# Kernel tuning notes

Measured on AMD Instinct MI355X. Metric: run time of the kernel, lower is better.

The kernel has to match this reference:

```python
import jax, jax.numpy as jnp
import numpy as np

H = 128          # input hidden dim
HID = 128        # expert hidden width
OUT = 128        # out_channels
NR = 8           # n_routed
NS = 2           # n_shared
RDIM = 16        # router feature dim


def setup_inputs() -> dict:
    key = jax.random.key(0)
    ks = jax.random.split(key, 11)
    s = 0.05
    x = jax.random.normal(ks[0], (2, 32, 32, 32, H), dtype=jnp.float32)
    # router params
    Wr1 = jax.random.normal(ks[1], (H, RDIM), dtype=jnp.float32) * s
    br1 = jnp.zeros((RDIM,), dtype=jnp.float32)
    Wr2 = jax.random.normal(ks[2], (RDIM, NR), dtype=jnp.float32) * s
    br2 = jnp.zeros((NR,), dtype=jnp.float32)
    # routed expert params, stacked on leading expert axis
    We1 = jax.random.normal(ks[3], (NR, H, HID), dtype=jnp.float32) * s
    be1 = jnp.zeros((NR, HID), dtype=jnp.float32)
    We2 = jax.random.normal(ks[4], (NR, HID, OUT), dtype=jnp.float32) * s
    be2 = jnp.zeros((NR, OUT), dtype=jnp.float32)
    # shared expert params
    Ws1 = jax.random.normal(ks[5], (NS, H, HID), dtype=jnp.float32) * s
    bs1 = jnp.zeros((NS, HID), dtype=jnp.float32)
    Ws2 = jax.random.normal(ks[6], (NS, HID, OUT), dtype=jnp.float32) * s
    bs2 = jnp.zeros((NS, OUT), dtype=jnp.float32)
    return dict(x=x, Wr1=Wr1, br1=br1, Wr2=Wr2, br2=br2,
                We1=We1, be1=be1, We2=We2, be2=be2,
                Ws1=Ws1, bs1=bs1, Ws2=Ws2, bs2=bs2)


def reference(x, Wr1, br1, Wr2, br2, We1, be1, We2, be2, Ws1, bs1, Ws2, bs2):
    # router: Dense(16) -> relu -> Dense(n_routed) -> softmax
    rf = jax.nn.relu(jnp.einsum('...h,hr->...r', x, Wr1) + br1)
    logits = jnp.einsum('...r,re->...e', rf, Wr2) + br2
    gate = jax.nn.softmax(logits, axis=-1)                      # [..., NR]
    threshold = 1.0 / NR
    mask = (gate > threshold).astype(gate.dtype)
    mg = gate * mask
    mg = mg / (jnp.sum(mg, axis=-1, keepdims=True) + 1e-8)
    # routed experts (batched over expert axis e): Dense -> gelu(tanh) -> Dense
    hr = jax.nn.gelu(jnp.einsum('...h,ehd->...ed', x, We1) + be1)   # [..., NR, HID]
    ro = jnp.einsum('...ed,edo->...eo', hr, We2) + be2              # [..., NR, OUT]
    routed_agg = jnp.einsum('...eo,...e->...o', ro, mg)
    # shared experts summed
    hs = jax.nn.gelu(jnp.einsum('...h,ehd->...ed', x, Ws1) + bs1)   # [..., NS, HID]
    so = jnp.einsum('...ed,edo->...eo', hs, Ws2) + bs2              # [..., NS, OUT]
    shared_agg = jnp.sum(so, axis=-2)
    return routed_agg + shared_agg
```

## Files before the change

### kernel.cpp

```cpp
#include <hip/hip_runtime.h>
#include <hip/hip_bf16.h>

typedef __bf16 bf16x8 __attribute__((ext_vector_type(8)));
typedef __bf16 bf16x4 __attribute__((ext_vector_type(4)));
typedef float  f32x16 __attribute__((ext_vector_type(16)));
typedef float  f32x4  __attribute__((ext_vector_type(4)));

static __device__ __forceinline__ f32x16 mfma32(bf16x8 a, bf16x8 b, f32x16 c) {
    return __builtin_amdgcn_mfma_f32_32x32x16_bf16(a, b, c, 0, 0, 0);
}

__global__ __launch_bounds__(256) void pack_kernel(
    const float* __restrict__ We1, const float* __restrict__ Ws1,
    const float* __restrict__ We2, const float* __restrict__ Ws2,
    __bf16* __restrict__ w1p, __bf16* __restrict__ w2p)
{
    int idx = blockIdx.x * 256 + threadIdx.x;
    int which = idx / 20480;
    int tid = idx - which * 20480;
    int l  = tid & 63;
    int ks = (tid >> 6) & 7;
    int nt = (tid >> 9) & 3;
    int e  = tid >> 11;
    const float* src;
    __bf16* dst;
    if (which == 0) {
        src = (e < 8) ? (We1 + e * 16384) : (Ws1 + (e - 8) * 16384);
        dst = w1p;
    } else {
        src = (e < 8) ? (We2 + e * 16384) : (Ws2 + (e - 8) * 16384);
        dst = w2p;
    }
    int col  = nt * 32 + (l & 31);
    int krow = ks * 16 + (l >> 5) * 8;
    bf16x8 v;
    #pragma unroll
    for (int j = 0; j < 8; ++j)
        v[j] = (__bf16)src[(krow + j) * 128 + col];
    *(bf16x8*)(dst + (((e * 4 + nt) * 8 + ks) * 64 + l) * 8) = v;
}

__global__ __launch_bounds__(256) void router_kernel(
    const float* __restrict__ x,
    const float* __restrict__ Wr1, const float* __restrict__ br1,
    const float* __restrict__ Wr2, const float* __restrict__ br2,
    float* __restrict__ mg)
{
    int tok = blockIdx.x * 256 + threadIdx.x;
    const float* xr = x + (size_t)tok * 128;
    double rf[16];
    #pragma unroll
    for (int r = 0; r < 16; ++r) rf[r] = (double)br1[r];
    #pragma unroll 4
    for (int k = 0; k < 128; ++k) {
        double xv = (double)xr[k];
        #pragma unroll
        for (int r = 0; r < 16; ++r)
            rf[r] = fma(xv, (double)Wr1[k * 16 + r], rf[r]);
    }
    #pragma unroll
    for (int r = 0; r < 16; ++r) rf[r] = rf[r] > 0.0 ? rf[r] : 0.0;
    double lg[8];
    #pragma unroll
    for (int j = 0; j < 8; ++j) lg[j] = (double)br2[j];
    #pragma unroll
    for (int r = 0; r < 16; ++r) {
        double rv = rf[r];
        #pragma unroll
        for (int j = 0; j < 8; ++j)
            lg[j] = fma(rv, (double)Wr2[r * 8 + j], lg[j]);
    }
    double mx = lg[0];
    #pragma unroll
    for (int j = 1; j < 8; ++j) mx = lg[j] > mx ? lg[j] : mx;
    double ex[8]; double s = 0.0;
    #pragma unroll
    for (int j = 0; j < 8; ++j) { ex[j] = exp(lg[j] - mx); s += ex[j]; }
    double mv[8]; double ms = 0.0;
    #pragma unroll
    for (int j = 0; j < 8; ++j) {
        double g = ex[j] / s;
        double m = (g > 0.125) ? g : 0.0;
        mv[j] = m; ms += m;
    }
    double inv = 1.0 / (ms + 1e-8);
    f32x4 o0, o1;
    o0[0]=(float)(mv[0]*inv); o0[1]=(float)(mv[1]*inv);
    o0[2]=(float)(mv[2]*inv); o0[3]=(float)(mv[3]*inv);
    o1[0]=(float)(mv[4]*inv); o1[1]=(float)(mv[5]*inv);
    o1[2]=(float)(mv[6]*inv); o1[3]=(float)(mv[7]*inv);
    f32x4* op = (f32x4*)(mg + (size_t)tok * 8);
    op[0] = o0; op[1] = o1;
}

__global__ __launch_bounds__(256, 2) void moe_main_kernel(
    const float* __restrict__ x, const float* __restrict__ mg,
    const __bf16* __restrict__ w1p, const __bf16* __restrict__ w2p,
    const float* __restrict__ be1, const float* __restrict__ bs1,
    const float* __restrict__ be2, const float* __restrict__ bs2,
    float* __restrict__ out)
{
    __shared__ __align__(16) __bf16 Xp[16384];
    __shared__ __align__(16) __bf16 Hp[16384];

    const int t    = threadIdx.x;
    const int lane = t & 63;
    const int wave = t >> 6;
    const int l31  = lane & 31;
    const int lh   = lane >> 5;
    const int tok0 = blockIdx.x * 128;
    const int ntp  = (wave & 1) * 2;
    const int mtp  = (wave >> 1) * 2;

    #pragma unroll
    for (int i = 0; i < 8; ++i) {
        int g = i * 256 + t;
        int m = g >> 4;
        int c = g & 15;
        const f32x4* srcp = (const f32x4*)(x + (size_t)(tok0 + m) * 128 + c * 8);
        f32x4 va = srcp[0], vb = srcp[1];
        bf16x8 v;
        v[0]=(__bf16)va[0]; v[1]=(__bf16)va[1]; v[2]=(__bf16)va[2]; v[3]=(__bf16)va[3];
        v[4]=(__bf16)vb[0]; v[5]=(__bf16)vb[1]; v[6]=(__bf16)vb[2]; v[7]=(__bf16)vb[3];
        *(bf16x8*)&Xp[(((m >> 5) * 8 + (c >> 1)) * 64 + (c & 1) * 32 + (m & 31)) * 8] = v;
    }
    __syncthreads();

    f32x16 acc[2][2];
    #pragma unroll
    for (int i0 = 0; i0 < 2; ++i0)
        #pragma unroll
        for (int i1 = 0; i1 < 2; ++i1)
            #pragma unroll
            for (int i = 0; i < 16; ++i) acc[i0][i1][i] = 0.f;

    #pragma unroll 1
    for (int e = 0; e < 10; ++e) {
        float gate0 = 1.f, gate1 = 1.f;
        if (e < 8) {
            gate0 = mg[(size_t)(tok0 + (mtp + 0) * 32 + l31) * 8 + e];
            gate1 = mg[(size_t)(tok0 + (mtp + 1) * 32 + l31) * 8 + e];
        }
        const float* b1p = (e < 8) ? (be1 + e * 128) : (bs1 + (e - 8) * 128);

        const __bf16* w1b = w1p + (size_t)e * 16384;
        bf16x8 wf[2][8];
        #pragma unroll
        for (int n2 = 0; n2 < 2; ++n2)
            #pragma unroll
            for (int ks = 0; ks < 8; ++ks)
                wf[n2][ks] = *(const bf16x8*)(w1b + (((ntp + n2) * 8 + ks) * 64 + lane) * 8);

        f32x16 a1[2][2];
        #pragma unroll
        for (int i0 = 0; i0 < 2; ++i0)
            #pragma unroll
            for (int i1 = 0; i1 < 2; ++i1)
                #pragma unroll
                for (int i = 0; i < 16; ++i) a1[i0][i1][i] = 0.f;

        #pragma unroll
        for (int ks = 0; ks < 8; ++ks) {
            bf16x8 xb0 = *(const bf16x8*)&Xp[(((mtp + 0) * 8 + ks) * 64 + lane) * 8];
            bf16x8 xb1 = *(const bf16x8*)&Xp[(((mtp + 1) * 8 + ks) * 64 + lane) * 8];
            a1[0][0] = mfma32(wf[0][ks], xb0, a1[0][0]);
            a1[0][1] = mfma32(wf[0][ks], xb1, a1[0][1]);
            a1[1][0] = mfma32(wf[1][ks], xb0, a1[1][0]);
            a1[1][1] = mfma32(wf[1][ks], xb1, a1[1][1]);
        }
        __syncthreads();

        #pragma unroll
        for (int n2 = 0; n2 < 2; ++n2) {
            const int ntile = ntp + n2;
            #pragma unroll
            for (int m2 = 0; m2 < 2; ++m2) {
                const int mtile = mtp + m2;
                const float gv = (m2 == 0) ? gate0 : gate1;
                #pragma unroll
                for (int gq = 0; gq < 4; ++gq) {
                    int n0 = ntile * 32 + gq * 8 + lh * 4;
                    f32x4 b1v = *(const f32x4*)(b1p + n0);
                    bf16x4 hv;
                    #pragma unroll
                    for (int q = 0; q < 4; ++q) {
                        float v = a1[n2][m2][gq * 4 + q] + b1v[q];
                        float u  = 1.5957691216f * fmaf(0.044715f * v, v * v, v);
                        float sg = 1.f / (1.f + __expf(-u));
                        hv[q] = (__bf16)(v * sg * gv);
                    }
                    *(bf16x4*)&Hp[((mtile * 8 + (n0 >> 4)) * 64 + ((n0 >> 3) & 1) * 32 + l31) * 8
                                  + (n0 & 7)] = hv;
                }
            }
        }
        __syncthreads();

        const __bf16* w2b = w2p + (size_t)e * 16384;
        #pragma unroll
        for (int o2 = 0; o2 < 2; ++o2)
            #pragma unroll
            for (int ks = 0; ks < 8; ++ks)
                wf[o2][ks] = *(const bf16x8*)(w2b + (((ntp + o2) * 8 + ks) * 64 + lane) * 8);

        #pragma unroll
        for (int ks = 0; ks < 8; ++ks) {
            bf16x8 h0 = *(const bf16x8*)&Hp[(((mtp + 0) * 8 + ks) * 64 + lane) * 8];
            bf16x8 h1 = *(const bf16x8*)&Hp[(((mtp + 1) * 8 + ks) * 64 + lane) * 8];
            acc[0][0] = mfma32(h0, wf[0][ks], acc[0][0]);
            acc[0][1] = mfma32(h0, wf[1][ks], acc[0][1]);
            acc[1][0] = mfma32(h1, wf[0][ks], acc[1][0]);
            acc[1][1] = mfma32(h1, wf[1][ks], acc[1][1]);
        }
    }

    float be2c[2][8], bs2c[2];
    #pragma unroll
    for (int o2 = 0; o2 < 2; ++o2) {
        int o = (ntp + o2) * 32 + l31;
        #pragma unroll
        for (int ee = 0; ee < 8; ++ee) be2c[o2][ee] = be2[ee * 128 + o];
        bs2c[o2] = bs2[o] + bs2[128 + o];
    }
    const float* mgb = mg + (size_t)tok0 * 8;
    #pragma unroll
    for (int m2 = 0; m2 < 2; ++m2) {
        int mtile = mtp + m2;
        #pragma unroll
        for (int rg = 0; rg < 16; ++rg) {
            int mloc = mtile * 32 + 4 * lh + (rg & 3) + 8 * (rg >> 2);
            f32x4 g0 = *(const f32x4*)&mgb[mloc * 8];
            f32x4 g1 = *(const f32x4*)&mgb[mloc * 8 + 4];
            #pragma unroll
            for (int o2 = 0; o2 < 2; ++o2) {
                float b = bs2c[o2];
                #pragma unroll
                for (int ee = 0; ee < 4; ++ee) b = fmaf(g0[ee], be2c[o2][ee], b);
                #pragma unroll
                for (int ee = 0; ee < 4; ++ee) b = fmaf(g1[ee], be2c[o2][4 + ee], b);
                out[(size_t)(tok0 + mloc) * 128 + (ntp + o2) * 32 + l31] =
                    acc[m2][o2][rg] + b;
            }
        }
    }
}

extern "C" void kernel_launch(void* const* d_in, const int* in_sizes, int n_in,
                              void* d_out, int out_size, void* d_ws, size_t ws_size,
                              hipStream_t stream)
{
    const float* x   = (const float*)d_in[0];
    const float* Wr1 = (const float*)d_in[1];
    const float* br1 = (const float*)d_in[2];
    const float* Wr2 = (const float*)d_in[3];
    const float* br2 = (const float*)d_in[4];
    const float* We1 = (const float*)d_in[5];
    const float* be1 = (const float*)d_in[6];
    const float* We2 = (const float*)d_in[7];
    const float* be2 = (const float*)d_in[8];
    const float* Ws1 = (const float*)d_in[9];
    const float* bs1 = (const float*)d_in[10];
    const float* Ws2 = (const float*)d_in[11];
    const float* bs2 = (const float*)d_in[12];

    __bf16* w1p = (__bf16*)d_ws;
    __bf16* w2p = (__bf16*)((char*)d_ws + 327680);
    float*  mg  = (float*)((char*)d_ws + 655360);

    pack_kernel<<<160, 256, 0, stream>>>(We1, Ws1, We2, Ws2, w1p, w2p);
    router_kernel<<<256, 256, 0, stream>>>(x, Wr1, br1, Wr2, br2, mg);
    moe_main_kernel<<<512, 256, 0, stream>>>(x, mg, w1p, w2p, be1, bs1, be2, bs2,
                                             (float*)d_out);
}
```

Before: 205.8 us.

## Keep expert hidden activations in registers, fold bias into GEMM, split hidden across waves

The main kernel now chains the two expert GEMMs in registers. The first GEMM's accumulator layout is fed straight into the second GEMM's A operand, which removes the hidden-activation LDS round trip and its two barriers per expert. The first-layer bias is folded in as an extra K slice (a ones column in X, a bias row in the packed weights). Each wave pair splits the hidden dimension and reduces partial outputs through LDS at the end. GELU switches to an exp2/rcp form, and the router stages x through LDS with smaller blocks. This trades an extra K step and a final cross-wave reduction for fewer syncs and less LDS traffic, with tiles halved to 64 tokens per block.

```diff
diff --git a/kernel.cpp b/kernel.cpp
--- a/kernel.cpp
+++ b/kernel.cpp
@@ -2,61 +2,93 @@
 #include <hip/hip_bf16.h>
 
 typedef __bf16 bf16x8 __attribute__((ext_vector_type(8)));
-typedef __bf16 bf16x4 __attribute__((ext_vector_type(4)));
 typedef float  f32x16 __attribute__((ext_vector_type(16)));
 typedef float  f32x4  __attribute__((ext_vector_type(4)));
+typedef float  f32x2  __attribute__((ext_vector_type(2)));
 
 static __device__ __forceinline__ f32x16 mfma32(bf16x8 a, bf16x8 b, f32x16 c) {
     return __builtin_amdgcn_mfma_f32_32x32x16_bf16(a, b, c, 0, 0, 0);
 }
 
+#define GELU_C1 2.30220820f
+#define GELU_C2 0.10294324f
+
 __global__ __launch_bounds__(256) void pack_kernel(
-    const float* __restrict__ We1, const float* __restrict__ Ws1,
+    const float* __restrict__ We1, const float* __restrict__ be1,
+    const float* __restrict__ Ws1, const float* __restrict__ bs1,
     const float* __restrict__ We2, const float* __restrict__ Ws2,
     __bf16* __restrict__ w1p, __bf16* __restrict__ w2p)
 {
-    int idx = blockIdx.x * 256 + threadIdx.x;
-    int which = idx / 20480;
-    int tid = idx - which * 20480;
-    int l  = tid & 63;
-    int ks = (tid >> 6) & 7;
-    int nt = (tid >> 9) & 3;
-    int e  = tid >> 11;
-    const float* src;
-    __bf16* dst;
-    if (which == 0) {
-        src = (e < 8) ? (We1 + e * 16384) : (Ws1 + (e - 8) * 16384);
-        dst = w1p;
-    } else {
-        src = (e < 8) ? (We2 + e * 16384) : (Ws2 + (e - 8) * 16384);
-        dst = w2p;
-    }
-    int col  = nt * 32 + (l & 31);
-    int krow = ks * 16 + (l >> 5) * 8;
-    bf16x8 v;
-    #pragma unroll
-    for (int j = 0; j < 8; ++j)
-        v[j] = (__bf16)src[(krow + j) * 128 + col];
-    *(bf16x8*)(dst + (((e * 4 + nt) * 8 + ks) * 64 + l) * 8) = v;
-}
-
-__global__ __launch_bounds__(256) void router_kernel(
+    int tid = blockIdx.x * 256 + threadIdx.x;
+    if (tid < 23040) {
+        int l  = tid & 63;
+        int ks = (tid >> 6) % 9;
+        int nt = (tid / 576) & 3;
+        int e  = tid / 2304;
+        const float* src = (e < 8) ? (We1 + e * 16384) : (Ws1 + (e - 8) * 16384);
+        const float* bia = (e < 8) ? (be1 + e * 128)   : (bs1 + (e - 8) * 128);
+        int n = nt * 32 + (l & 31);
+        int kb = ks * 16 + (l >> 5) * 8;
+        bf16x8 v;
+        #pragma unroll
+        for (int j = 0; j < 8; ++j) {
+            int k = kb + j;
+            float f = (k < 128) ? src[k * 128 + n] : ((k == 128) ? bia[n] : 0.f);
+            v[j] = (__bf16)f;
+        }
+        *(bf16x8*)(w1p + (size_t)tid * 8) = v;
+    } else if (tid < 43520) {
+        int t2 = tid - 23040;
+        int l  = t2 & 63;
+        int ks = (t2 >> 6) & 7;
+        int ot = (t2 / 512) & 3;
+        int e  = t2 / 2048;
+        const float* src = (e < 8) ? (We2 + e * 16384) : (Ws2 + (e - 8) * 16384);
+        int o  = ot * 32 + (l & 31);
+        int lh = l >> 5;
+        bf16x8 v;
+        #pragma unroll
+        for (int j = 0; j < 8; ++j) {
+            int hid = 16 * ks + 8 * (j >> 2) + 4 * lh + (j & 3);
+            v[j] = (__bf16)src[hid * 128 + o];
+        }
+        *(bf16x8*)(w2p + (size_t)t2 * 8) = v;
+    }
+}
+
+__global__ __launch_bounds__(64) void router_kernel(
     const float* __restrict__ x,
     const float* __restrict__ Wr1, const float* __restrict__ br1,
     const float* __restrict__ Wr2, const float* __restrict__ br2,
     float* __restrict__ mg)
 {
-    int tok = blockIdx.x * 256 + threadIdx.x;
-    const float* xr = x + (size_t)tok * 128;
+    __shared__ __align__(16) float xs[64 * 132];
+    int t = threadIdx.x;
+    size_t base = (size_t)blockIdx.x * 64 * 128;
+    #pragma unroll 4
+    for (int i = 0; i < 32; ++i) {
+        int idx = i * 64 + t;
+        f32x4 v = *(const f32x4*)(x + base + (size_t)idx * 4);
+        int m = (idx * 4) >> 7;
+        int c = (idx * 4) & 127;
+        *(f32x4*)&xs[m * 132 + c] = v;
+    }
+    __syncthreads();
+
+    const f32x4* xr = (const f32x4*)(xs + t * 132);
     double rf[16];
     #pragma unroll
     for (int r = 0; r < 16; ++r) rf[r] = (double)br1[r];
-    #pragma unroll 4
-    for (int k = 0; k < 128; ++k) {
-        double xv = (double)xr[k];
-        #pragma unroll
-        for (int r = 0; r < 16; ++r)
-            rf[r] = fma(xv, (double)Wr1[k * 16 + r], rf[r]);
+    for (int c = 0; c < 32; ++c) {
+        f32x4 xv4 = xr[c];
+        #pragma unroll
+        for (int q = 0; q < 4; ++q) {
+            double xv = (double)xv4[q];
+            int k = c * 4 + q;
+            #pragma unroll
+            for (int r = 0; r < 16; ++r)
+                rf[r] = fma(xv, (double)Wr1[k * 16 + r], rf[r]);
+        }
     }
     #pragma unroll
     for (int r = 0; r < 16; ++r) rf[r] = rf[r] > 0.0 ? rf[r] : 0.0;
@@ -84,6 +116,7 @@
         mv[j] = m; ms += m;
     }
     double inv = 1.0 / (ms + 1e-8);
+    int tok = blockIdx.x * 64 + t;
     f32x4 o0, o1;
     o0[0]=(float)(mv[0]*inv); o0[1]=(float)(mv[1]*inv);
     o0[2]=(float)(mv[2]*inv); o0[3]=(float)(mv[3]*inv);
@@ -96,150 +129,152 @@
 __global__ __launch_bounds__(256, 2) void moe_main_kernel(
     const float* __restrict__ x, const float* __restrict__ mg,
     const __bf16* __restrict__ w1p, const __bf16* __restrict__ w2p,
-    const float* __restrict__ be1, const float* __restrict__ bs1,
     const float* __restrict__ be2, const float* __restrict__ bs2,
     float* __restrict__ out)
 {
-    __shared__ __align__(16) __bf16 Xp[16384];
-    __shared__ __align__(16) __bf16 Hp[16384];
+    __shared__ __align__(16) char lds[32768];
+    __bf16* Xp = (__bf16*)lds;
+    float*  Red = (float*)lds;
 
     const int t    = threadIdx.x;
     const int lane = t & 63;
     const int wave = t >> 6;
     const int l31  = lane & 31;
     const int lh   = lane >> 5;
-    const int tok0 = blockIdx.x * 128;
-    const int ntp  = (wave & 1) * 2;
-    const int mtp  = (wave >> 1) * 2;
-
-    #pragma unroll
-    for (int i = 0; i < 8; ++i) {
+    const int mt   = wave >> 1;
+    const int h    = wave & 1;
+    const int tok0 = blockIdx.x * 64;
+
+    #pragma unroll
+    for (int i = 0; i < 4; ++i) {
         int g = i * 256 + t;
         int m = g >> 4;
         int c = g & 15;
-        const f32x4* srcp = (const f32x4*)(x + (size_t)(tok0 + m) * 128 + c * 8);
-        f32x4 va = srcp[0], vb = srcp[1];
+        const f32x4* sp = (const f32x4*)(x + (size_t)(tok0 + m) * 128 + c * 8);
+        f32x4 va = sp[0], vb = sp[1];
         bf16x8 v;
         v[0]=(__bf16)va[0]; v[1]=(__bf16)va[1]; v[2]=(__bf16)va[2]; v[3]=(__bf16)va[3];
         v[4]=(__bf16)vb[0]; v[5]=(__bf16)vb[1]; v[6]=(__bf16)vb[2]; v[7]=(__bf16)vb[3];
-        *(bf16x8*)&Xp[(((m >> 5) * 8 + (c >> 1)) * 64 + (c & 1) * 32 + (m & 31)) * 8] = v;
+        *(bf16x8*)&Xp[(((m >> 5) * 9 + (c >> 1)) * 64 + (c & 1) * 32 + (m & 31)) * 8] = v;
+    }
+    if (t < 128) {
+        int mtx = t >> 6, l = t & 63;
+        bf16x8 v;
+        #pragma unroll
+        for (int j = 0; j < 8; ++j) v[j] = (__bf16)0.f;
+        if (l < 32) v[0] = (__bf16)1.0f;
+        *(bf16x8*)&Xp[((mtx * 9 + 8) * 64 + l) * 8] = v;
     }
     __syncthreads();
 
-    f32x16 acc[2][2];
-    #pragma unroll
-    for (int i0 = 0; i0 < 2; ++i0)
-        #pragma unroll
-        for (int i1 = 0; i1 < 2; ++i1)
-            #pragma unroll
-            for (int i = 0; i < 16; ++i) acc[i0][i1][i] = 0.f;
+    const float* mgr = mg + (size_t)(tok0 + 32 * mt + l31) * 8;
+    f32x4 ga4 = *(const f32x4*)mgr;
+    f32x4 gb4 = *(const f32x4*)(mgr + 4);
+    float gte[8] = {ga4[0], ga4[1], ga4[2], ga4[3], gb4[0], gb4[1], gb4[2], gb4[3]};
+
+    f32x16 acc[4];
+    #pragma unroll
+    for (int ot = 0; ot < 4; ++ot)
+        #pragma unroll
+        for (int i = 0; i < 16; ++i) acc[ot][i] = 0.f;
+
+    const bf16x8* w1v = (const bf16x8*)w1p;
+    const bf16x8* w2v = (const bf16x8*)w2p;
 
     #pragma unroll 1
     for (int e = 0; e < 10; ++e) {
-        float gate0 = 1.f, gate1 = 1.f;
-        if (e < 8) {
-            gate0 = mg[(size_t)(tok0 + (mtp + 0) * 32 + l31) * 8 + e];
-            gate1 = mg[(size_t)(tok0 + (mtp + 1) * 32 + l31) * 8 + e];
-        }
-        const float* b1p = (e < 8) ? (be1 + e * 128) : (bs1 + (e - 8) * 128);
-
-        const __bf16* w1b = w1p + (size_t)e * 16384;
-        bf16x8 wf[2][8];
+        const bf16x8* wap = w1v + ((size_t)(e * 4 + 2 * h) * 9) * 64 + lane;
+        bf16x8 wa[9], wb[9];
+        #pragma unroll
+        for (int ks = 0; ks < 9; ++ks) { wa[ks] = wap[ks * 64]; wb[ks] = wap[(9 + ks) * 64]; }
+
+        f32x16 a1[2];
         #pragma unroll
         for (int n2 = 0; n2 < 2; ++n2)
             #pragma unroll
-            for (int ks = 0; ks < 8; ++ks)
-                wf[n2][ks] = *(const bf16x8*)(w1b + (((ntp + n2) * 8 + ks) * 64 + lane) * 8);
-
-        f32x16 a1[2][2];
-        #pragma unroll
-        for (int i0 = 0; i0 < 2; ++i0)
-            #pragma unroll
-            for (int i1 = 0; i1 < 2; ++i1)
+            for (int i = 0; i < 16; ++i) a1[n2][i] = 0.f;
+
+        #pragma unroll
+        for (int ks = 0; ks < 9; ++ks) {
+            bf16x8 xb = *(const bf16x8*)&Xp[((mt * 9 + ks) * 64 + lane) * 8];
+            a1[0] = mfma32(wa[ks], xb, a1[0]);
+            a1[1] = mfma32(wb[ks], xb, a1[1]);
+        }
+
+        const bf16x8* wBp = w2v + ((size_t)(e * 4) * 8 + 4 * h) * 64 + lane;
+        bf16x8 wB[4][4];
+        #pragma unroll
+        for (int ot = 0; ot < 4; ++ot)
+            #pragma unroll
+            for (int kq = 0; kq < 4; ++kq)
+                wB[ot][kq] = wBp[(ot * 8 + kq) * 64];
+
+        const float gv = (e < 8) ? gte[e] : 1.0f;
+
+        #pragma unroll
+        for (int n2 = 0; n2 < 2; ++n2) {
+            #pragma unroll
+            for (int b = 0; b < 2; ++b) {
+                bf16x8 fr;
                 #pragma unroll
-                for (int i = 0; i < 16; ++i) a1[i0][i1][i] = 0.f;
-
-        #pragma unroll
-        for (int ks = 0; ks < 8; ++ks) {
-            bf16x8 xb0 = *(const bf16x8*)&Xp[(((mtp + 0) * 8 + ks) * 64 + lane) * 8];
-            bf16x8 xb1 = *(const bf16x8*)&Xp[(((mtp + 1) * 8 + ks) * 64 + lane) * 8];
-            a1[0][0] = mfma32(wf[0][ks], xb0, a1[0][0]);
-            a1[0][1] = mfma32(wf[0][ks], xb1, a1[0][1]);
-            a1[1][0] = mfma32(wf[1][ks], xb0, a1[1][0]);
-            a1[1][1] = mfma32(wf[1][ks], xb1, a1[1][1]);
-        }
-        __syncthreads();
-
-        #pragma unroll
-        for (int n2 = 0; n2 < 2; ++n2) {
-            const int ntile = ntp + n2;
-            #pragma unroll
-            for (int m2 = 0; m2 < 2; ++m2) {
-                const int mtile = mtp + m2;
-                const float gv = (m2 == 0) ? gate0 : gate1;
+                for (int jp = 0; jp < 4; ++jp) {
+                    f32x2 hh; hh[0] = a1[n2][8 * b + 2 * jp]; hh[1] = a1[n2][8 * b + 2 * jp + 1];
+                    f32x2 tt = hh * hh;
+                    f32x2 pp;
+                    pp[0] = fmaf(tt[0], -GELU_C2, -GELU_C1);
+                    pp[1] = fmaf(tt[1], -GELU_C2, -GELU_C1);
+                    f32x2 mm = hh * pp;
+                    float e0 = __builtin_amdgcn_exp2f(mm[0]);
+                    float e1 = __builtin_amdgcn_exp2f(mm[1]);
+                    float q0 = __builtin_amdgcn_rcpf(1.f + e0);
+                    float q1 = __builtin_amdgcn_rcpf(1.f + e1);
+                    f32x2 gg; gg[0] = hh[0] * q0 * gv; gg[1] = hh[1] * q1 * gv;
+                    fr[2 * jp]     = (__bf16)gg[0];
+                    fr[2 * jp + 1] = (__bf16)gg[1];
+                }
+                int kq = 2 * n2 + b;
+                acc[0] = mfma32(fr, wB[0][kq], acc[0]);
+                acc[1] = mfma32(fr, wB[1][kq], acc[1]);
+                acc[2] = mfma32(fr, wB[2][kq], acc[2]);
+                acc[3] = mfma32(fr, wB[3][kq], acc[3]);
+            }
+        }
+    }
+
+    __syncthreads();
+    if (h == 1) {
+        #pragma unroll
+        for (int ot = 0; ot < 4; ++ot)
+            #pragma unroll
+            for (int r = 0; r < 16; ++r)
+                Red[((mt * 4 + ot) * 16 + r) * 64 + lane] = acc[ot][r];
+    }
+    __syncthreads();
+    if (h == 0) {
+        float be2c[4][8], bsc[4];
+        #pragma unroll
+        for (int ot = 0; ot < 4; ++ot) {
+            int o = 32 * ot + l31;
+            bsc[ot] = bs2[o] + bs2[128 + o];
+            #pragma unroll
+            for (int ee = 0; ee < 8; ++ee) be2c[ot][ee] = be2[ee * 128 + o];
+        }
+        const float* mgb = mg + (size_t)(tok0 + 32 * mt) * 8;
+        #pragma unroll
+        for (int r = 0; r < 16; ++r) {
+            int mrow = (r & 3) + 8 * (r >> 2) + 4 * lh;
+            f32x4 g0 = *(const f32x4*)&mgb[mrow * 8];
+            f32x4 g1 = *(const f32x4*)&mgb[mrow * 8 + 4];
+            size_t orow = (size_t)(tok0 + 32 * mt + mrow) * 128;
+            #pragma unroll
+            for (int ot = 0; ot < 4; ++ot) {
+                float b = bsc[ot];
                 #pragma unroll
-                for (int gq = 0; gq < 4; ++gq) {
-                    int n0 = ntile * 32 + gq * 8 + lh * 4;
-                    f32x4 b1v = *(const f32x4*)(b1p + n0);
-                    bf16x4 hv;
-                    #pragma unroll
-                    for (int q = 0; q < 4; ++q) {
-                        float v = a1[n2][m2][gq * 4 + q] + b1v[q];
-                        float u  = 1.5957691216f * fmaf(0.044715f * v, v * v, v);
-                        float sg = 1.f / (1.f + __expf(-u));
-                        hv[q] = (__bf16)(v * sg * gv);
-                    }
-                    *(bf16x4*)&Hp[((mtile * 8 + (n0 >> 4)) * 64 + ((n0 >> 3) & 1) * 32 + l31) * 8
-                                  + (n0 & 7)] = hv;
-                }
-            }
-        }
-        __syncthreads();
-
-        const __bf16* w2b = w2p + (size_t)e * 16384;
-        #pragma unroll
-        for (int o2 = 0; o2 < 2; ++o2)
-            #pragma unroll
-            for (int ks = 0; ks < 8; ++ks)
-                wf[o2][ks] = *(const bf16x8*)(w2b + (((ntp + o2) * 8 + ks) * 64 + lane) * 8);
-
-        #pragma unroll
-        for (int ks = 0; ks < 8; ++ks) {
-            bf16x8 h0 = *(const bf16x8*)&Hp[(((mtp + 0) * 8 + ks) * 64 + lane) * 8];
-            bf16x8 h1 = *(const bf16x8*)&Hp[(((mtp + 1) * 8 + ks) * 64 + lane) * 8];
-            acc[0][0] = mfma32(h0, wf[0][ks], acc[0][0]);
-            acc[0][1] = mfma32(h0, wf[1][ks], acc[0][1]);
-            acc[1][0] = mfma32(h1, wf[0][ks], acc[1][0]);
-            acc[1][1] = mfma32(h1, wf[1][ks], acc[1][1]);
-        }
-    }
-
-    float be2c[2][8], bs2c[2];
-    #pragma unroll
-    for (int o2 = 0; o2 < 2; ++o2) {
-        int o = (ntp + o2) * 32 + l31;
-        #pragma unroll
-        for (int ee = 0; ee < 8; ++ee) be2c[o2][ee] = be2[ee * 128 + o];
-        bs2c[o2] = bs2[o] + bs2[128 + o];
-    }
-    const float* mgb = mg + (size_t)tok0 * 8;
-    #pragma unroll
-    for (int m2 = 0; m2 < 2; ++m2) {
-        int mtile = mtp + m2;
-        #pragma unroll
-        for (int rg = 0; rg < 16; ++rg) {
-            int mloc = mtile * 32 + 4 * lh + (rg & 3) + 8 * (rg >> 2);
-            f32x4 g0 = *(const f32x4*)&mgb[mloc * 8];
-            f32x4 g1 = *(const f32x4*)&mgb[mloc * 8 + 4];
-            #pragma unroll
-            for (int o2 = 0; o2 < 2; ++o2) {
-                float b = bs2c[o2];
+                for (int ee = 0; ee < 4; ++ee) b = fmaf(g0[ee], be2c[ot][ee], b);
                 #pragma unroll
-                for (int ee = 0; ee < 4; ++ee) b = fmaf(g0[ee], be2c[o2][ee], b);
-                #pragma unroll
-                for (int ee = 0; ee < 4; ++ee) b = fmaf(g1[ee], be2c[o2][4 + ee], b);
-                out[(size_t)(tok0 + mloc) * 128 + (ntp + o2) * 32 + l31] =
-                    acc[m2][o2][rg] + b;
+                for (int ee = 0; ee < 4; ++ee) b = fmaf(g1[ee], be2c[ot][4 + ee], b);
+                float v = acc[ot][r] + Red[((mt * 4 + ot) * 16 + r) * 64 + lane] + b;
+                out[orow + 32 * ot + l31] = v;
             }
         }
     }
@@ -264,11 +299,11 @@
     const float* bs2 = (const float*)d_in[12];
 
     __bf16* w1p = (__bf16*)d_ws;
-    __bf16* w2p = (__bf16*)((char*)d_ws + 327680);
-    float*  mg  = (float*)((char*)d_ws + 655360);
-
-    pack_kernel<<<160, 256, 0, stream>>>(We1, Ws1, We2, Ws2, w1p, w2p);
-    router_kernel<<<256, 256, 0, stream>>>(x, Wr1, br1, Wr2, br2, mg);
-    moe_main_kernel<<<512, 256, 0, stream>>>(x, mg, w1p, w2p, be1, bs1, be2, bs2,
-                                             (float*)d_out);
-}
+    __bf16* w2p = (__bf16*)((char*)d_ws + 368640);
+    float*  mg  = (float*)((char*)d_ws + 696320);
+
+    pack_kernel<<<170, 256, 0, stream>>>(We1, be1, Ws1, bs1, We2, Ws2, w1p, w2p);
+    router_kernel<<<1024, 64, 0, stream>>>(x, Wr1, br1, Wr2, br2, mg);
+    moe_main_kernel<<<1024, 256, 0, stream>>>(x, mg, w1p, w2p, be2, bs2,
+                                              (float*)d_out);
+}
```

New measurement: 197.0 us. 1.04x faster.
